# Performance work log

Hardware: AMD Instinct MI355X
Metric: run time of the kernel (lower is better)

The kernel has to match this reference:

```python
import jax, jax.numpy as jnp
import numpy as np

B, L, LM_DIM, D, R, NUM_LAYERS, C = 32, 1024, 1024, 128, 3, 2, 8
N = B * L
E = 524288
LN_EPS = 1e-5


def setup_inputs() -> dict:
    key = jax.random.key(0)
    ks = jax.random.split(key, 16)
    inp = {
        'output': jax.random.normal(ks[0], (B, L, LM_DIM), dtype=jnp.float32),
        'edge_index': jax.random.randint(ks[1], (2, E), 0, N, dtype=jnp.int64),
        'edge_type': jax.random.randint(ks[2], (E,), 0, R, dtype=jnp.int64),
        'attention_mask': jax.random.randint(ks[3], (B, L), 0, 2, dtype=jnp.int64),
        'labels': jax.random.randint(ks[4], (B, L), 0, C, dtype=jnp.int64),
        # parameters
        'lm_W': jax.random.normal(ks[5], (D, LM_DIM), dtype=jnp.float32) * 0.02,
        'lm_b': jnp.zeros((D,), dtype=jnp.float32),
        'ln_g': jnp.ones((D,), dtype=jnp.float32),
        'ln_b': jnp.zeros((D,), dtype=jnp.float32),
        'W_rel': jax.random.normal(ks[6], (NUM_LAYERS, R, D, D), dtype=jnp.float32) * 0.05,
        'W_root': jax.random.normal(ks[7], (NUM_LAYERS, D, D), dtype=jnp.float32) * 0.05,
        'conv_b': jnp.zeros((NUM_LAYERS, D), dtype=jnp.float32),
        'cls_W': jax.random.normal(ks[8], (C, 2 * D), dtype=jnp.float32) * 0.05,
        'cls_b': jnp.zeros((C,), dtype=jnp.float32),
    }
    return inp


def _forward(output, edge_index, edge_type, attention_mask, labels,
             lm_W, lm_b, ln_g, ln_b, W_rel, W_root, conv_b, cls_W, cls_b):
    # LM head + ReLU (dropout is identity in eval) + LayerNorm
    lm = jax.nn.relu(jnp.einsum('bld,hd->blh', output, lm_W) + lm_b)
    mu = jnp.mean(lm, axis=-1, keepdims=True)
    var = jnp.mean(jnp.square(lm - mu), axis=-1, keepdims=True)
    lm = (lm - mu) * jax.lax.rsqrt(var + LN_EPS) * ln_g + ln_b  # [B,L,D]

    # RGCN over flattened nodes
    x = lm.reshape(N, D)
    src, dst = edge_index[0], edge_index[1]
    seg = dst * R + edge_type  # combined (node, relation) segment id
    ones = jnp.ones((E,), dtype=x.dtype)
    cnt = jax.ops.segment_sum(ones, seg, num_segments=N * R).reshape(N, R, 1)
    denom = jnp.maximum(cnt, 1.0)
    for layer in range(NUM_LAYERS):
        x_src = x[src]  # [E,D] gather
        sums = jax.ops.segment_sum(x_src, seg, num_segments=N * R).reshape(N, R, D)
        mean_r = sums / denom  # per-relation mean aggregation (PyG RGCNConv aggr='mean')
        out = jnp.einsum('nrd,rde->ne', mean_r, W_rel[layer])
        out = out + x @ W_root[layer] + conv_b[layer]
        x = jax.nn.relu(out)  # dropout identity

    g = x.reshape(B, L, D)
    feat = jnp.concatenate([lm, g], axis=-1)  # [B,L,2D]
    logits = jnp.einsum('blh,ch->blc', feat, cls_W) + cls_b  # [B,L,C]

    # masked cross-entropy (ignore where attention_mask != 1)
    valid = (attention_mask.reshape(-1) == 1)
    logp = jax.nn.log_softmax(logits.reshape(-1, C), axis=-1)
    nll = -jnp.take_along_axis(logp, labels.reshape(-1, 1), axis=1)[:, 0]
    n_valid = jnp.maximum(jnp.sum(valid.astype(logits.dtype)), 1.0)
    loss = jnp.sum(jnp.where(valid, nll, 0.0)) / n_valid
    return loss, logits


def reference(output, edge_index, edge_type, attention_mask, labels,
              lm_W, lm_b, ln_g, ln_b, W_rel, W_root, conv_b, cls_W, cls_b):
    return _forward(output, edge_index, edge_type, attention_mask, labels,
                    lm_W, lm_b, ln_g, ln_b, W_rel, W_root, conv_b, cls_W, cls_b)
```

## Files before the change

kernel.cpp:

```cpp
#include <hip/hip_runtime.h>

#define Bb 32
#define Ll 1024
#define LMD 1024
#define Dd 128
#define Rr 3
#define NLAYER 2
#define Cc 8
#define Nn (Bb*Ll)
#define Ee 524288
#define NSEG (Nn*Rr)
#define LN_EPS 1e-5f

typedef __attribute__((ext_vector_type(8))) short bf16x8;
typedef __attribute__((ext_vector_type(4))) float f32x4;

__device__ inline short f2bf(float f) {
    unsigned u = __builtin_bit_cast(unsigned, f);
    u += 0x7fff + ((u >> 16) & 1);
    return (short)(u >> 16);
}
__device__ inline float bf2f(unsigned short s) {
    unsigned u = ((unsigned)s) << 16;
    return __builtin_bit_cast(float, u);
}

__global__ __launch_bounds__(256) void pack_all_kernel(
    const float* __restrict__ lmW, const float* __restrict__ Wrel,
    const float* __restrict__ Wroot, short* __restrict__ Wp_all)
{
    int idx = blockIdx.x * 256 + threadIdx.x;
    float v;
    if (idx < 131072) {
        int kk = idx & 31, n = (idx >> 5) & 127, ks = idx >> 12;
        v = lmW[n * 1024 + ks * 32 + kk];
    } else {
        int j = idx - 131072;
        int layer = j >> 16;
        int kk = j & 31, n = (j >> 5) & 127, ks = (j >> 12) & 15;
        int k = ks * 32 + kk;
        v = (k < 384) ? Wrel[(size_t)layer * 49152 + (size_t)k * 128 + n]
                      : Wroot[(size_t)layer * 16384 + (size_t)(k - 384) * 128 + n];
    }
    Wp_all[idx] = f2bf(v);
}

__global__ __launch_bounds__(256) void lm_gemm_ln_kernel(
    const float* __restrict__ A,
    const short* __restrict__ Wp,
    const float* __restrict__ bias,
    const float* __restrict__ lng, const float* __restrict__ lnb,
    float* __restrict__ lm_f32, short* __restrict__ lm_bf16)
{
    const int wv   = threadIdx.x >> 6;
    const int lane = threadIdx.x & 63;
    const int m16  = lane & 15;
    const int quad = lane >> 4;
    const int row_frag = blockIdx.x * 64 + wv * 16 + m16;
    const float* arow = A + (size_t)row_frag * 1024 + quad * 8;

    f32x4 acc[8];
    #pragma unroll
    for (int i = 0; i < 8; ++i) acc[i] = (f32x4){0.f, 0.f, 0.f, 0.f};

    #pragma unroll 2
    for (int ks = 0; ks < 32; ++ks) {
        const short* wpb = Wp + ks * 4096 + m16 * 32 + quad * 8;
        bf16x8 bfr[8];
        #pragma unroll
        for (int nt = 0; nt < 8; ++nt)
            bfr[nt] = *(const bf16x8*)(wpb + nt * 512);
        const float4* ap = (const float4*)(arow + ks * 32);
        float4 a0 = ap[0], a1 = ap[1];
        union { bf16x8 v; short s[8]; } af;
        af.s[0] = f2bf(a0.x); af.s[1] = f2bf(a0.y);
        af.s[2] = f2bf(a0.z); af.s[3] = f2bf(a0.w);
        af.s[4] = f2bf(a1.x); af.s[5] = f2bf(a1.y);
        af.s[6] = f2bf(a1.z); af.s[7] = f2bf(a1.w);
        #pragma unroll
        for (int nt = 0; nt < 8; ++nt)
            acc[nt] = __builtin_amdgcn_mfma_f32_16x16x32_bf16(af.v, bfr[nt], acc[nt], 0, 0, 0);
    }

    float v[8][4];
    #pragma unroll
    for (int nt = 0; nt < 8; ++nt) {
        float bs = bias[nt * 16 + m16];
        #pragma unroll
        for (int r = 0; r < 4; ++r) v[nt][r] = fmaxf(acc[nt][r] + bs, 0.f);
    }
    float gv[8], bv[8];
    #pragma unroll
    for (int nt = 0; nt < 8; ++nt) { gv[nt] = lng[nt * 16 + m16]; bv[nt] = lnb[nt * 16 + m16]; }

    const int row0 = blockIdx.x * 64 + wv * 16 + quad * 4;
    #pragma unroll
    for (int r = 0; r < 4; ++r) {
        float s = 0.f;
        #pragma unroll
        for (int nt = 0; nt < 8; ++nt) s += v[nt][r];
        s += __shfl_xor(s, 1, 64); s += __shfl_xor(s, 2, 64);
        s += __shfl_xor(s, 4, 64); s += __shfl_xor(s, 8, 64);
        float mu = s * (1.f / 128.f);
        float q = 0.f;
        #pragma unroll
        for (int nt = 0; nt < 8; ++nt) { float d = v[nt][r] - mu; q += d * d; }
        q += __shfl_xor(q, 1, 64); q += __shfl_xor(q, 2, 64);
        q += __shfl_xor(q, 4, 64); q += __shfl_xor(q, 8, 64);
        float rs = rsqrtf(q * (1.f / 128.f) + LN_EPS);
        size_t rowoff = (size_t)(row0 + r) * 128;
        #pragma unroll
        for (int nt = 0; nt < 8; ++nt) {
            float o = (v[nt][r] - mu) * rs * gv[nt] + bv[nt];
            lm_f32[rowoff + nt * 16 + m16] = o;
            lm_bf16[rowoff + nt * 16 + m16] = f2bf(o);
        }
    }
}

__global__ __launch_bounds__(256) void conv_gemm_kernel(
    const short* __restrict__ A1,
    const short* __restrict__ A2,
    const short* __restrict__ Wp,
    const float* __restrict__ bias,
    short* __restrict__ out_bf16)
{
    const int wv   = threadIdx.x >> 6;
    const int lane = threadIdx.x & 63;
    const int m16  = lane & 15;
    const int quad = lane >> 4;
    const int row_frag = blockIdx.x * 64 + wv * 16 + m16;
    const short* a1row = A1 + (size_t)row_frag * 384 + quad * 8;
    const short* a2row = A2 + (size_t)row_frag * 128 + quad * 8;

    f32x4 acc[8];
    #pragma unroll
    for (int i = 0; i < 8; ++i) acc[i] = (f32x4){0.f, 0.f, 0.f, 0.f};

    #pragma unroll 2
    for (int ks = 0; ks < 16; ++ks) {
        const short* wpb = Wp + ks * 4096 + m16 * 32 + quad * 8;
        bf16x8 bfr[8];
        #pragma unroll
        for (int nt = 0; nt < 8; ++nt)
            bfr[nt] = *(const bf16x8*)(wpb + nt * 512);
        const short* ar = (ks < 12) ? (a1row + ks * 32) : (a2row + (ks - 12) * 32);
        bf16x8 af = *(const bf16x8*)ar;
        #pragma unroll
        for (int nt = 0; nt < 8; ++nt)
            acc[nt] = __builtin_amdgcn_mfma_f32_16x16x32_bf16(af, bfr[nt], acc[nt], 0, 0, 0);
    }

    const int row0 = blockIdx.x * 64 + wv * 16 + quad * 4;
    #pragma unroll
    for (int nt = 0; nt < 8; ++nt) {
        float bs = bias[nt * 16 + m16];
        #pragma unroll
        for (int r = 0; r < 4; ++r) {
            float o = fmaxf(acc[nt][r] + bs, 0.f);
            out_bf16[(size_t)(row0 + r) * 128 + nt * 16 + m16] = f2bf(o);
        }
    }
}

__global__ __launch_bounds__(256) void hist_kernel(
    const int* __restrict__ dst, const int* __restrict__ et, int* __restrict__ counts)
{
    int e = blockIdx.x * 256 + threadIdx.x;
    atomicAdd(&counts[dst[e] * 3 + et[e]], 1);
}

__global__ __launch_bounds__(256) void scan_blk_kernel(
    const int* __restrict__ counts, int* __restrict__ excl, int* __restrict__ blksum)
{
    __shared__ int wsum[4];
    int t = threadIdx.x, lane = t & 63, wv = t >> 6;
    int g = blockIdx.x * 256 + t;
    int v = counts[g];
    int x = v;
    #pragma unroll
    for (int off = 1; off < 64; off <<= 1) {
        int y = __shfl_up(x, off, 64);
        if (lane >= off) x += y;
    }
    if (lane == 63) wsum[wv] = x;
    __syncthreads();
    int woff = 0;
    for (int i = 0; i < wv; ++i) woff += wsum[i];
    excl[g] = woff + x - v;
    if (t == 255) blksum[blockIdx.x] = woff + x;
}

__global__ __launch_bounds__(512) void scan_top_kernel(
    const int* __restrict__ blksum, int* __restrict__ blkoff)
{
    __shared__ int wsum[8];
    int t = threadIdx.x, lane = t & 63, wv = t >> 6;
    int v = (t < 384) ? blksum[t] : 0;
    int x = v;
    #pragma unroll
    for (int off = 1; off < 64; off <<= 1) {
        int y = __shfl_up(x, off, 64);
        if (lane >= off) x += y;
    }
    if (lane == 63) wsum[wv] = x;
    __syncthreads();
    int woff = 0;
    for (int i = 0; i < wv; ++i) woff += wsum[i];
    if (t < 384) blkoff[t] = woff + x - v;
}

__global__ __launch_bounds__(256) void scan_add_kernel(
    const int* __restrict__ excl, const int* __restrict__ blkoff, int* __restrict__ row_ptr)
{
    int g = blockIdx.x * 256 + threadIdx.x;
    row_ptr[g] = excl[g] + blkoff[blockIdx.x];
    if (g == 0) row_ptr[NSEG] = Ee;
}

__global__ __launch_bounds__(256) void scatter_kernel(
    const int* __restrict__ src, const int* __restrict__ dst, const int* __restrict__ et,
    const int* __restrict__ row_ptr, int* __restrict__ fill, int* __restrict__ edge_src)
{
    int e = blockIdx.x * 256 + threadIdx.x;
    int s = dst[e] * 3 + et[e];
    int pos = row_ptr[s] + atomicAdd(&fill[s], 1);
    edge_src[pos] = src[e];
}

__global__ __launch_bounds__(256) void aggregate_kernel(
    const short* __restrict__ x, const int* __restrict__ row_ptr,
    const int* __restrict__ edge_src, short* __restrict__ agg)
{
    int seg  = blockIdx.x * 4 + (threadIdx.x >> 6);
    int lane = threadIdx.x & 63;
    int b = row_ptr[seg], e = row_ptr[seg + 1];
    int n = seg / 3, r = seg - n * 3;
    float ax = 0.f, ay = 0.f;
    int i = b;
    for (; i + 2 <= e; i += 2) {
        int s0 = edge_src[i], s1 = edge_src[i + 1];
        unsigned u0 = *(const unsigned*)(x + (size_t)s0 * 128 + lane * 2);
        unsigned u1 = *(const unsigned*)(x + (size_t)s1 * 128 + lane * 2);
        ax += bf2f((unsigned short)(u0 & 0xffff)) + bf2f((unsigned short)(u1 & 0xffff));
        ay += bf2f((unsigned short)(u0 >> 16))    + bf2f((unsigned short)(u1 >> 16));
    }
    if (i < e) {
        int s0 = edge_src[i];
        unsigned u0 = *(const unsigned*)(x + (size_t)s0 * 128 + lane * 2);
        ax += bf2f((unsigned short)(u0 & 0xffff));
        ay += bf2f((unsigned short)(u0 >> 16));
    }
    int cnt = e - b;
    float inv = 1.f / (float)(cnt > 0 ? cnt : 1);
    unsigned short lo = (unsigned short)f2bf(ax * inv);
    unsigned short hi = (unsigned short)f2bf(ay * inv);
    *(unsigned*)(agg + (size_t)n * 384 + r * 128 + lane * 2) = (unsigned)lo | ((unsigned)hi << 16);
}

__global__ __launch_bounds__(256) void cls_loss_kernel(
    const float* __restrict__ lm, const short* __restrict__ g,
    const float* __restrict__ clsW, const float* __restrict__ clsb,
    const int* __restrict__ mask, const int* __restrict__ labels,
    float* __restrict__ logits, float* __restrict__ accb)
{
    __shared__ float W[2048];
    for (int i = threadIdx.x; i < 2048; i += 256) W[i] = clsW[i];
    __syncthreads();
    int n = blockIdx.x * 256 + threadIdx.x;
    float l[8];
    #pragma unroll
    for (int c = 0; c < 8; ++c) l[c] = clsb[c];
    const float* lmr = lm + (size_t)n * 128;
    const short* gr  = g  + (size_t)n * 128;
    #pragma unroll 4
    for (int h = 0; h < 128; h += 4) {
        float4 a = *(const float4*)(lmr + h);
        #pragma unroll
        for (int c = 0; c < 8; ++c) {
            const float* w = &W[c * 256 + h];
            l[c] = fmaf(a.x, w[0], l[c]); l[c] = fmaf(a.y, w[1], l[c]);
            l[c] = fmaf(a.z, w[2], l[c]); l[c] = fmaf(a.w, w[3], l[c]);
        }
    }
    #pragma unroll 2
    for (int h = 0; h < 128; h += 8) {
        uint4 raw = *(const uint4*)(gr + h);
        float a[8];
        a[0] = bf2f((unsigned short)(raw.x & 0xffff)); a[1] = bf2f((unsigned short)(raw.x >> 16));
        a[2] = bf2f((unsigned short)(raw.y & 0xffff)); a[3] = bf2f((unsigned short)(raw.y >> 16));
        a[4] = bf2f((unsigned short)(raw.z & 0xffff)); a[5] = bf2f((unsigned short)(raw.z >> 16));
        a[6] = bf2f((unsigned short)(raw.w & 0xffff)); a[7] = bf2f((unsigned short)(raw.w >> 16));
        #pragma unroll
        for (int c = 0; c < 8; ++c) {
            const float* w = &W[c * 256 + 128 + h];
            #pragma unroll
            for (int j = 0; j < 8; ++j) l[c] = fmaf(a[j], w[j], l[c]);
        }
    }
    #pragma unroll
    for (int c = 0; c < 8; ++c) logits[(size_t)n * 8 + c] = l[c];

    float m = l[0];
    #pragma unroll
    for (int c = 1; c < 8; ++c) m = fmaxf(m, l[c]);
    float ss = 0.f;
    #pragma unroll
    for (int c = 0; c < 8; ++c) ss += expf(l[c] - m);
    float lse = m + logf(ss);
    int y = labels[n];
    float ly = l[0];
    #pragma unroll
    for (int c = 1; c < 8; ++c) ly = (y == c) ? l[c] : ly;
    float nll = lse - ly;
    bool valid = (mask[n] == 1);
    float lv = valid ? nll : 0.f;
    float cv = valid ? 1.f : 0.f;
    #pragma unroll
    for (int off = 32; off > 0; off >>= 1) {
        lv += __shfl_down(lv, off, 64);
        cv += __shfl_down(cv, off, 64);
    }
    if ((threadIdx.x & 63) == 0) { atomicAdd(&accb[0], lv); atomicAdd(&accb[1], cv); }
}

__global__ void finalize_kernel(const float* __restrict__ accb, float* __restrict__ out)
{
    out[0] = accb[0] / fmaxf(accb[1], 1.f);
}

extern "C" void kernel_launch(void* const* d_in, const int* in_sizes, int n_in,
                              void* d_out, int out_size, void* d_ws, size_t ws_size,
                              hipStream_t stream)
{
    const float* output = (const float*)d_in[0];
    const int* edge_index = (const int*)d_in[1];
    const int* edge_type  = (const int*)d_in[2];
    const int* attn       = (const int*)d_in[3];
    const int* labels     = (const int*)d_in[4];
    const float* lmW   = (const float*)d_in[5];
    const float* lmb   = (const float*)d_in[6];
    const float* lng   = (const float*)d_in[7];
    const float* lnb   = (const float*)d_in[8];
    const float* Wrel  = (const float*)d_in[9];
    const float* Wroot = (const float*)d_in[10];
    const float* convb = (const float*)d_in[11];
    const float* clsW  = (const float*)d_in[12];
    const float* clsb  = (const float*)d_in[13];

    char* ws = (char*)d_ws;
    float* lm_f32 = (float*)ws;                          ws += (size_t)Nn * Dd * 4;
    short* lm_bf  = (short*)ws;                          ws += (size_t)Nn * Dd * 2;
    short* x1_bf  = (short*)ws;                          ws += (size_t)Nn * Dd * 2;
    short* x2_bf  = (short*)ws;                          ws += (size_t)Nn * Dd * 2;
    short* agg_bf = (short*)ws;                          ws += (size_t)Nn * 384 * 2;
    short* Wp_all = (short*)ws;                          ws += (size_t)262144 * 2;
    float* accb   = (float*)ws;                          ws += 64;
    int* counts   = (int*)ws;                            ws += (size_t)NSEG * 4;
    int* fill     = (int*)ws;                            ws += (size_t)NSEG * 4;
    int* row_ptr  = (int*)ws;                            ws += (size_t)(NSEG + 4) * 4;
    int* excl     = (int*)ws;                            ws += (size_t)NSEG * 4;
    int* blksum   = (int*)ws;                            ws += 512 * 4;
    int* blkoff   = (int*)ws;                            ws += 512 * 4;
    int* edge_src = (int*)ws;

    short* Wp_lm = Wp_all;
    short* Wp_c0 = Wp_all + 131072;
    short* Wp_c1 = Wp_all + 131072 + 65536;

    const int* e_src = edge_index;
    const int* e_dst = edge_index + Ee;

    hipMemsetAsync(accb, 0, 64 + 2 * (size_t)NSEG * 4, stream);

    pack_all_kernel<<<dim3(1024), dim3(256), 0, stream>>>(lmW, Wrel, Wroot, Wp_all);

    lm_gemm_ln_kernel<<<dim3(Nn / 64), dim3(256), 0, stream>>>(
        output, Wp_lm, lmb, lng, lnb, lm_f32, lm_bf);

    hist_kernel<<<dim3(Ee / 256), dim3(256), 0, stream>>>(e_dst, edge_type, counts);
    scan_blk_kernel<<<dim3(NSEG / 256), dim3(256), 0, stream>>>(counts, excl, blksum);
    scan_top_kernel<<<dim3(1), dim3(512), 0, stream>>>(blksum, blkoff);
    scan_add_kernel<<<dim3(NSEG / 256), dim3(256), 0, stream>>>(excl, blkoff, row_ptr);
    scatter_kernel<<<dim3(Ee / 256), dim3(256), 0, stream>>>(
        e_src, e_dst, edge_type, row_ptr, fill, edge_src);

    aggregate_kernel<<<dim3(NSEG / 4), dim3(256), 0, stream>>>(lm_bf, row_ptr, edge_src, agg_bf);
    conv_gemm_kernel<<<dim3(Nn / 64), dim3(256), 0, stream>>>(
        agg_bf, lm_bf, Wp_c0, convb, x1_bf);
    aggregate_kernel<<<dim3(NSEG / 4), dim3(256), 0, stream>>>(x1_bf, row_ptr, edge_src, agg_bf);
    conv_gemm_kernel<<<dim3(Nn / 64), dim3(256), 0, stream>>>(
        agg_bf, x1_bf, Wp_c1, convb + Dd, x2_bf);

    float* logits = (float*)d_out + 1;
    cls_loss_kernel<<<dim3(Nn / 256), dim3(256), 0, stream>>>(
        lm_f32, x2_bf, clsW, clsb, attn, labels, logits, accb);
    finalize_kernel<<<dim3(1), dim3(1), 0, stream>>>(accb, (float*)d_out);
}
```

Baseline: 455.6 us.

## Merge small kernels, drop fp32 LM copy, unroll gather, fold loss finalize

Measured after the change: 438.5 us. 1.04x faster.

```diff
diff --git a/kernel.cpp b/kernel.cpp
--- a/kernel.cpp
+++ b/kernel.cpp
@@ -25,24 +25,32 @@
     return __builtin_bit_cast(float, u);
 }
 
-__global__ __launch_bounds__(256) void pack_all_kernel(
+__global__ __launch_bounds__(256) void prep_kernel(
     const float* __restrict__ lmW, const float* __restrict__ Wrel,
-    const float* __restrict__ Wroot, short* __restrict__ Wp_all)
-{
-    int idx = blockIdx.x * 256 + threadIdx.x;
-    float v;
-    if (idx < 131072) {
-        int kk = idx & 31, n = (idx >> 5) & 127, ks = idx >> 12;
-        v = lmW[n * 1024 + ks * 32 + kk];
+    const float* __restrict__ Wroot, short* __restrict__ Wp_all,
+    const int* __restrict__ dst, const int* __restrict__ et,
+    int* __restrict__ counts)
+{
+    int bid = blockIdx.x;
+    if (bid < 1024) {
+        int idx = bid * 256 + threadIdx.x;
+        float v;
+        if (idx < 131072) {
+            int kk = idx & 31, n = (idx >> 5) & 127, ks = idx >> 12;
+            v = lmW[n * 1024 + ks * 32 + kk];
+        } else {
+            int j = idx - 131072;
+            int layer = j >> 16;
+            int kk = j & 31, n = (j >> 5) & 127, ks = (j >> 12) & 15;
+            int k = ks * 32 + kk;
+            v = (k < 384) ? Wrel[(size_t)layer * 49152 + (size_t)k * 128 + n]
+                          : Wroot[(size_t)layer * 16384 + (size_t)(k - 384) * 128 + n];
+        }
+        Wp_all[idx] = f2bf(v);
     } else {
-        int j = idx - 131072;
-        int layer = j >> 16;
-        int kk = j & 31, n = (j >> 5) & 127, ks = (j >> 12) & 15;
-        int k = ks * 32 + kk;
-        v = (k < 384) ? Wrel[(size_t)layer * 49152 + (size_t)k * 128 + n]
-                      : Wroot[(size_t)layer * 16384 + (size_t)(k - 384) * 128 + n];
-    }
-    Wp_all[idx] = f2bf(v);
+        int e = (bid - 1024) * 256 + threadIdx.x;
+        atomicAdd(&counts[dst[e] * 3 + et[e]], 1);
+    }
 }
 
 __global__ __launch_bounds__(256) void lm_gemm_ln_kernel(
@@ -50,7 +58,7 @@
     const short* __restrict__ Wp,
     const float* __restrict__ bias,
     const float* __restrict__ lng, const float* __restrict__ lnb,
-    float* __restrict__ lm_f32, short* __restrict__ lm_bf16)
+    short* __restrict__ lm_bf16)
 {
     const int wv   = threadIdx.x >> 6;
     const int lane = threadIdx.x & 63;
@@ -112,7 +120,6 @@
         #pragma unroll
         for (int nt = 0; nt < 8; ++nt) {
             float o = (v[nt][r] - mu) * rs * gv[nt] + bv[nt];
-            lm_f32[rowoff + nt * 16 + m16] = o;
             lm_bf16[rowoff + nt * 16 + m16] = f2bf(o);
         }
     }
@@ -163,13 +170,6 @@
     }
 }
 
-__global__ __launch_bounds__(256) void hist_kernel(
-    const int* __restrict__ dst, const int* __restrict__ et, int* __restrict__ counts)
-{
-    int e = blockIdx.x * 256 + threadIdx.x;
-    atomicAdd(&counts[dst[e] * 3 + et[e]], 1);
-}
-
 __global__ __launch_bounds__(256) void scan_blk_kernel(
     const int* __restrict__ counts, int* __restrict__ excl, int* __restrict__ blksum)
 {
@@ -191,30 +191,23 @@
     if (t == 255) blksum[blockIdx.x] = woff + x;
 }
 
-__global__ __launch_bounds__(512) void scan_top_kernel(
-    const int* __restrict__ blksum, int* __restrict__ blkoff)
-{
-    __shared__ int wsum[8];
-    int t = threadIdx.x, lane = t & 63, wv = t >> 6;
-    int v = (t < 384) ? blksum[t] : 0;
-    int x = v;
-    #pragma unroll
-    for (int off = 1; off < 64; off <<= 1) {
-        int y = __shfl_up(x, off, 64);
-        if (lane >= off) x += y;
-    }
-    if (lane == 63) wsum[wv] = x;
+__global__ __launch_bounds__(256) void scan_add_kernel(
+    const int* __restrict__ excl, const int* __restrict__ blksum,
+    int* __restrict__ row_ptr)
+{
+    __shared__ int ws4[4];
+    __shared__ int off_sh;
+    const int t = threadIdx.x, bid = blockIdx.x;
+    int s = 0;
+    for (int j = t; j < bid; j += 256) s += blksum[j];
+    #pragma unroll
+    for (int o = 32; o > 0; o >>= 1) s += __shfl_xor(s, o, 64);
+    if ((t & 63) == 0) ws4[t >> 6] = s;
     __syncthreads();
-    int woff = 0;
-    for (int i = 0; i < wv; ++i) woff += wsum[i];
-    if (t < 384) blkoff[t] = woff + x - v;
-}
-
-__global__ __launch_bounds__(256) void scan_add_kernel(
-    const int* __restrict__ excl, const int* __restrict__ blkoff, int* __restrict__ row_ptr)
-{
-    int g = blockIdx.x * 256 + threadIdx.x;
-    row_ptr[g] = excl[g] + blkoff[blockIdx.x];
+    if (t == 0) off_sh = ws4[0] + ws4[1] + ws4[2] + ws4[3];
+    __syncthreads();
+    int g = bid * 256 + t;
+    row_ptr[g] = excl[g] + off_sh;
     if (g == 0) row_ptr[NSEG] = Ee;
 }
 
@@ -238,6 +231,18 @@
     int n = seg / 3, r = seg - n * 3;
     float ax = 0.f, ay = 0.f;
     int i = b;
+    for (; i + 4 <= e; i += 4) {
+        int s0 = edge_src[i],     s1 = edge_src[i + 1];
+        int s2 = edge_src[i + 2], s3 = edge_src[i + 3];
+        unsigned u0 = *(const unsigned*)(x + (size_t)s0 * 128 + lane * 2);
+        unsigned u1 = *(const unsigned*)(x + (size_t)s1 * 128 + lane * 2);
+        unsigned u2 = *(const unsigned*)(x + (size_t)s2 * 128 + lane * 2);
+        unsigned u3 = *(const unsigned*)(x + (size_t)s3 * 128 + lane * 2);
+        ax += bf2f((unsigned short)(u0 & 0xffff)) + bf2f((unsigned short)(u1 & 0xffff))
+            + bf2f((unsigned short)(u2 & 0xffff)) + bf2f((unsigned short)(u3 & 0xffff));
+        ay += bf2f((unsigned short)(u0 >> 16)) + bf2f((unsigned short)(u1 >> 16))
+            + bf2f((unsigned short)(u2 >> 16)) + bf2f((unsigned short)(u3 >> 16));
+    }
     for (; i + 2 <= e; i += 2) {
         int s0 = edge_src[i], s1 = edge_src[i + 1];
         unsigned u0 = *(const unsigned*)(x + (size_t)s0 * 128 + lane * 2);
@@ -259,10 +264,11 @@
 }
 
 __global__ __launch_bounds__(256) void cls_loss_kernel(
-    const float* __restrict__ lm, const short* __restrict__ g,
+    const short* __restrict__ lm, const short* __restrict__ g,
     const float* __restrict__ clsW, const float* __restrict__ clsb,
     const int* __restrict__ mask, const int* __restrict__ labels,
-    float* __restrict__ logits, float* __restrict__ accb)
+    float* __restrict__ logits, float* __restrict__ accb,
+    unsigned* __restrict__ ticket, float* __restrict__ loss_out)
 {
     __shared__ float W[2048];
     for (int i = threadIdx.x; i < 2048; i += 256) W[i] = clsW[i];
@@ -271,16 +277,21 @@
     float l[8];
     #pragma unroll
     for (int c = 0; c < 8; ++c) l[c] = clsb[c];
-    const float* lmr = lm + (size_t)n * 128;
+    const short* lmr = lm + (size_t)n * 128;
     const short* gr  = g  + (size_t)n * 128;
-    #pragma unroll 4
-    for (int h = 0; h < 128; h += 4) {
-        float4 a = *(const float4*)(lmr + h);
+    #pragma unroll 2
+    for (int h = 0; h < 128; h += 8) {
+        uint4 raw = *(const uint4*)(lmr + h);
+        float a[8];
+        a[0] = bf2f((unsigned short)(raw.x & 0xffff)); a[1] = bf2f((unsigned short)(raw.x >> 16));
+        a[2] = bf2f((unsigned short)(raw.y & 0xffff)); a[3] = bf2f((unsigned short)(raw.y >> 16));
+        a[4] = bf2f((unsigned short)(raw.z & 0xffff)); a[5] = bf2f((unsigned short)(raw.z >> 16));
+        a[6] = bf2f((unsigned short)(raw.w & 0xffff)); a[7] = bf2f((unsigned short)(raw.w >> 16));
         #pragma unroll
         for (int c = 0; c < 8; ++c) {
             const float* w = &W[c * 256 + h];
-            l[c] = fmaf(a.x, w[0], l[c]); l[c] = fmaf(a.y, w[1], l[c]);
-            l[c] = fmaf(a.z, w[2], l[c]); l[c] = fmaf(a.w, w[3], l[c]);
+            #pragma unroll
+            for (int j = 0; j < 8; ++j) l[c] = fmaf(a[j], w[j], l[c]);
         }
     }
     #pragma unroll 2
@@ -322,11 +333,16 @@
         cv += __shfl_down(cv, off, 64);
     }
     if ((threadIdx.x & 63) == 0) { atomicAdd(&accb[0], lv); atomicAdd(&accb[1], cv); }
-}
-
-__global__ void finalize_kernel(const float* __restrict__ accb, float* __restrict__ out)
-{
-    out[0] = accb[0] / fmaxf(accb[1], 1.f);
+
+    __threadfence();
+    if (threadIdx.x == 0) {
+        unsigned t = atomicAdd(ticket, 1u);
+        if (t == gridDim.x - 1) {
+            float lsum = atomicAdd(&accb[0], 0.f);
+            float csum = atomicAdd(&accb[1], 0.f);
+            loss_out[0] = lsum / fmaxf(csum, 1.f);
+        }
+    }
 }
 
 extern "C" void kernel_launch(void* const* d_in, const int* in_sizes, int n_in,
@@ -349,7 +365,6 @@
     const float* clsb  = (const float*)d_in[13];
 
     char* ws = (char*)d_ws;
-    float* lm_f32 = (float*)ws;                          ws += (size_t)Nn * Dd * 4;
     short* lm_bf  = (short*)ws;                          ws += (size_t)Nn * Dd * 2;
     short* x1_bf  = (short*)ws;                          ws += (size_t)Nn * Dd * 2;
     short* x2_bf  = (short*)ws;                          ws += (size_t)Nn * Dd * 2;
@@ -361,8 +376,9 @@
     int* row_ptr  = (int*)ws;                            ws += (size_t)(NSEG + 4) * 4;
     int* excl     = (int*)ws;                            ws += (size_t)NSEG * 4;
     int* blksum   = (int*)ws;                            ws += 512 * 4;
-    int* blkoff   = (int*)ws;                            ws += 512 * 4;
     int* edge_src = (int*)ws;
+
+    unsigned* ticket = (unsigned*)(accb + 2);
 
     short* Wp_lm = Wp_all;
     short* Wp_c0 = Wp_all + 131072;
@@ -373,15 +389,14 @@
 
     hipMemsetAsync(accb, 0, 64 + 2 * (size_t)NSEG * 4, stream);
 
-    pack_all_kernel<<<dim3(1024), dim3(256), 0, stream>>>(lmW, Wrel, Wroot, Wp_all);
+    prep_kernel<<<dim3(1024 + Ee / 256), dim3(256), 0, stream>>>(
+        lmW, Wrel, Wroot, Wp_all, e_dst, edge_type, counts);
 
     lm_gemm_ln_kernel<<<dim3(Nn / 64), dim3(256), 0, stream>>>(
-        output, Wp_lm, lmb, lng, lnb, lm_f32, lm_bf);
-
-    hist_kernel<<<dim3(Ee / 256), dim3(256), 0, stream>>>(e_dst, edge_type, counts);
+        output, Wp_lm, lmb, lng, lnb, lm_bf);
+
     scan_blk_kernel<<<dim3(NSEG / 256), dim3(256), 0, stream>>>(counts, excl, blksum);
-    scan_top_kernel<<<dim3(1), dim3(512), 0, stream>>>(blksum, blkoff);
-    scan_add_kernel<<<dim3(NSEG / 256), dim3(256), 0, stream>>>(excl, blkoff, row_ptr);
+    scan_add_kernel<<<dim3(NSEG / 256), dim3(256), 0, stream>>>(excl, blksum, row_ptr);
     scatter_kernel<<<dim3(Ee / 256), dim3(256), 0, stream>>>(
         e_src, e_dst, edge_type, row_ptr, fill, edge_src);
 
@@ -394,6 +409,5 @@
 
     float* logits = (float*)d_out + 1;
     cls_loss_kernel<<<dim3(Nn / 256), dim3(256), 0, stream>>>(
-        lm_f32, x2_bf, clsW, clsb, attn, labels, logits, accb);
-    finalize_kernel<<<dim3(1), dim3(1), 0, stream>>>(accb, (float*)d_out);
-}
+        lm_bf, x2_bf, clsW, clsb, attn, labels, logits, accb, ticket, (float*)d_out);
+}
```
